# Performance work log

Hardware: AMD Instinct MI355X
Metric: run time of the kernel (lower is better)

The kernel has to match this reference:

```python
import jax, jax.numpy as jnp
import numpy as np

E = 768      # embed_dim (hidden_size)
H = 12       # num_attention_heads
DH = E // H  # head_dim = 64
B, S = 8, 1024


def setup_inputs() -> dict:
    key = jax.random.key(0)
    ks = jax.random.split(key, 10)
    sc = 1.0 / np.sqrt(E)
    inp = {
        "hidden_state": jax.random.normal(ks[0], (B, S, E), dtype=jnp.float32),
        # per-head Q/K/V projections, stacked over heads: [H, E, DH]
        "Wq": jax.random.normal(ks[1], (H, E, DH), dtype=jnp.float32) * sc,
        "bq": jax.random.normal(ks[2], (H, DH), dtype=jnp.float32) * 0.02,
        "Wk": jax.random.normal(ks[3], (H, E, DH), dtype=jnp.float32) * sc,
        "bk": jax.random.normal(ks[4], (H, DH), dtype=jnp.float32) * 0.02,
        "Wv": jax.random.normal(ks[5], (H, E, DH), dtype=jnp.float32) * sc,
        "bv": jax.random.normal(ks[6], (H, DH), dtype=jnp.float32) * 0.02,
        # output projection: [E, E]
        "Wo": jax.random.normal(ks[7], (E, E), dtype=jnp.float32) * sc,
        "bo": jax.random.normal(ks[8], (E,), dtype=jnp.float32) * 0.02,
    }
    return inp


def reference(hidden_state, Wq, bq, Wk, bk, Wv, bv, Wo, bo):
    # Q/K/V per head: [B,S,E] x [H,E,D] -> [B,H,S,D]
    q = jnp.einsum("bse,hed->bhsd", hidden_state, Wq) + bq[None, :, None, :]
    k = jnp.einsum("bse,hed->bhsd", hidden_state, Wk) + bk[None, :, None, :]
    v = jnp.einsum("bse,hed->bhsd", hidden_state, Wv) + bv[None, :, None, :]
    scale = 1.0 / jnp.sqrt(jnp.asarray(DH, dtype=q.dtype))
    scores = jnp.einsum("bhsd,bhtd->bhst", q, k) * scale   # [B,H,S,S]
    weights = jax.nn.softmax(scores, axis=-1)
    attn = jnp.einsum("bhst,bhtd->bhsd", weights, v)        # [B,H,S,D]
    # concat heads (head order matches ModuleList concat): [B,S,H*D]=[B,S,E]
    x = attn.transpose(0, 2, 1, 3).reshape(hidden_state.shape[0], hidden_state.shape[1], E)
    return x @ Wo + bo
```

## Files before the change

kernel.cpp:

```cpp
#include <hip/hip_runtime.h>

typedef unsigned short u16;
typedef __bf16 bf16;
typedef bf16 bf16x8 __attribute__((ext_vector_type(8)));
typedef float f32x4 __attribute__((ext_vector_type(4)));
typedef u16 u16x4 __attribute__((ext_vector_type(4)));
typedef u16 u16x8 __attribute__((ext_vector_type(8)));

#define MROWS 8192
#define EDIM 768
#define NQKV 2304
#define NHEAD 12
#define DH 64
#define SEQ 1024
#define BATCH 8
#define BH 96
#define BHSD (BH * SEQ * DH)
#define KIT64 (EDIM / 64)

#if __has_builtin(__builtin_amdgcn_exp2f)
#define EXP2(x) __builtin_amdgcn_exp2f(x)
#else
#define EXP2(x) exp2f(x)
#endif

__device__ __forceinline__ u16 f2bf(float f) {
  bf16 b = (bf16)f;
  return __builtin_bit_cast(u16, b);
}


__global__ void cvt_x(const float* __restrict__ x, u16* __restrict__ xb, int n) {
  int i = (blockIdx.x * blockDim.x + threadIdx.x) * 4;
  if (i >= n) return;
  float4 v = *(const float4*)(x + i);
  u16x4 o;
  o[0] = f2bf(v.x); o[1] = f2bf(v.y); o[2] = f2bf(v.z); o[3] = f2bf(v.w);
  *(u16x4*)(xb + i) = o;
}

__global__ __launch_bounds__(256) void pack_w(
    const float* __restrict__ Wq, const float* __restrict__ Wk,
    const float* __restrict__ Wv, const float* __restrict__ Wo,
    u16* __restrict__ Wt, u16* __restrict__ Wot) {
  __shared__ float T[64][65];
  int bid = blockIdx.x;
  int tid = threadIdx.x;
  int c = tid & 63, r4 = tid >> 6;
  if (bid < 432) {
    int region = bid / 144, rem = bid - region * 144;
    int h = rem / 12, e0 = (rem - h * 12) * 64;
    const float* W = region == 0 ? Wq : (region == 1 ? Wk : Wv);
    for (int p = 0; p < 16; p++) {
      int er = r4 + p * 4;
      T[er][c] = W[(size_t)(h * EDIM + e0 + er) * DH + c];
    }
    __syncthreads();
    int nbase = region * EDIM + h * 64;
    for (int p = 0; p < 16; p++) {
      int dr = r4 + p * 4;
      Wt[(size_t)(nbase + dr) * EDIM + e0 + c] = f2bf(T[c][dr]);
    }
  } else {
    bid -= 432;
    int n0 = (bid / 12) * 64, e0 = (bid - (bid / 12) * 12) * 64;
    for (int p = 0; p < 16; p++) {
      int er = r4 + p * 4;
      T[er][c] = Wo[(size_t)(e0 + er) * EDIM + n0 + c];
    }
    __syncthreads();
    for (int p = 0; p < 16; p++) {
      int dr = r4 + p * 4;
      Wot[(size_t)(n0 + dr) * EDIM + e0 + c] = f2bf(T[c][dr]);
    }
  }
}

__device__ __forceinline__ void gemm_core64(
    const u16* __restrict__ A, const u16* __restrict__ Bt,
    u16* As, u16* Bs,
    int m0, int n0, int tid, f32x4 acc[4][4]) {
  int wv = __builtin_amdgcn_readfirstlane(tid >> 6);
  int lane = tid & 63, quad = lane >> 4, l16 = lane & 15;
  int wm = (wv & 1) * 64, wn = (wv >> 1) * 64;
  int srow = tid >> 1;
  int cb = (tid & 1) * 4;
  const u16* Ag = A + (size_t)(m0 + srow) * EDIM + cb * 8;
  const u16* Bg = Bt + (size_t)(n0 + srow) * EDIM + cb * 8;
  int wbase = srow * 64;

  u16x8 ra[4], rb[4];
  for (int q = 0; q < 4; q++) {
    ra[q] = *(const u16x8*)(Ag + q * 8);
    rb[q] = *(const u16x8*)(Bg + q * 8);
  }
  for (int k = 0; k < KIT64; k++) {
    __syncthreads();
    for (int q = 0; q < 4; q++) {
      int sc = (((cb + q) ^ (srow & 7))) * 8;
      *(u16x8*)(As + wbase + sc) = ra[q];
      *(u16x8*)(Bs + wbase + sc) = rb[q];
    }
    __syncthreads();
    if (k + 1 < KIT64) {
      int ko = (k + 1) * 64;
      for (int q = 0; q < 4; q++) {
        ra[q] = *(const u16x8*)(Ag + ko + q * 8);
        rb[q] = *(const u16x8*)(Bg + ko + q * 8);
      }
    }
    for (int kh = 0; kh < 2; kh++) {
      bf16x8 af[4], bfr[4];
      for (int i = 0; i < 4; i++) {
        int row = wm + i * 16 + l16;
        af[i] = *(const bf16x8*)(As + row * 64 + (((kh * 4 + quad) ^ (row & 7))) * 8);
      }
      for (int j = 0; j < 4; j++) {
        int row = wn + j * 16 + l16;
        bfr[j] = *(const bf16x8*)(Bs + row * 64 + (((kh * 4 + quad) ^ (row & 7))) * 8);
      }
      for (int i = 0; i < 4; i++)
        for (int j = 0; j < 4; j++)
          acc[i][j] = __builtin_amdgcn_mfma_f32_16x16x32_bf16(af[i], bfr[j], acc[i][j], 0, 0, 0);
    }
  }
}

__global__ __launch_bounds__(256, 3) void gemm_qkv(
    const u16* __restrict__ A, const u16* __restrict__ Bt,
    const float* __restrict__ bq, const float* __restrict__ bk, const float* __restrict__ bv,
    u16* __restrict__ qkv) {
  __shared__ u16 As[128 * 64];
  __shared__ u16 Bs[128 * 64];
  int tid = threadIdx.x;
  int wv = tid >> 6, lane = tid & 63, quad = lane >> 4, l16 = lane & 15;
  int wm = (wv & 1) * 64, wn = (wv >> 1) * 64;
  int m0 = blockIdx.x * 128, n0 = blockIdx.y * 128;
  f32x4 acc[4][4] = {};
  gemm_core64(A, Bt, As, Bs, m0, n0, tid, acc);

  const float kQscale = 0.18033688011112042f;
  for (int i = 0; i < 4; i++) {
    int row0 = m0 + wm + i * 16 + quad * 4;
    for (int j = 0; j < 4; j++) {
      int n = n0 + wn + j * 16 + l16;
      int region = n / EDIM;
      int hd = n - region * EDIM;
      int h = hd >> 6, d = hd & 63;
      const float* bp = region == 0 ? bq : (region == 1 ? bk : bv);
      float bias = bp[hd];
      float scale = region == 0 ? kQscale : 1.0f;
      for (int r = 0; r < 4; r++) {
        int rr = row0 + r;
        int bb = rr >> 10, s = rr & 1023;
        float val = (acc[i][j][r] + bias) * scale;
        u16 bv16 = f2bf(val);
        int bhh = bb * NHEAD + h;
        if (region < 2) {
          qkv[(size_t)region * BHSD + ((size_t)bhh * SEQ + s) * DH + d] = bv16;
        } else {
          qkv[(size_t)2 * BHSD + ((size_t)bhh * DH + d) * SEQ + s] = bv16;
        }
      }
    }
  }
}

__global__ __launch_bounds__(256, 4) void attn_kernel(const u16* __restrict__ qkv, u16* __restrict__ attn) {
  int bh = blockIdx.x;
  int b = bh / NHEAD, h = bh - b * NHEAD;
  const u16* Q  = qkv + (size_t)bh * SEQ * DH;
  const u16* K  = qkv + (size_t)(BH + bh) * SEQ * DH;
  const u16* VT = qkv + (size_t)(2 * BH + bh) * SEQ * DH;
  int tid = threadIdx.x, wave = tid >> 6, lane = tid & 63, quad = lane >> 4, l16 = lane & 15;
  int q_base = blockIdx.y * 64 + wave * 16;

  __shared__ u16 Ks[64 * 72];
  __shared__ u16 Vts[80 * 72];
  __shared__ u16 Ps[4][16 * 72];

  for (int i = tid; i < 16 * 64; i += 256) {
    int rr = i >> 6, cc = i & 63;
    Vts[(64 + rr) * 72 + cc] = (rr == 0) ? (u16)0x3F80 : (u16)0;
  }

  bf16x8 qf[2];
  for (int c = 0; c < 2; c++)
    qf[c] = *(const bf16x8*)(Q + (size_t)(q_base + l16) * DH + c * 32 + quad * 8);

  f32x4 o[4] = {};
  f32x4 o5 = {};

  int tr = tid >> 3, tc8 = (tid & 7) * 8;

  u16x8 kv0 = *(const u16x8*)(K + (size_t)tr * DH + tc8);
  u16x8 kv1 = *(const u16x8*)(K + (size_t)(32 + tr) * DH + tc8);
  u16x8 vv0 = *(const u16x8*)(VT + (size_t)tr * SEQ + tc8);
  u16x8 vv1 = *(const u16x8*)(VT + (size_t)(32 + tr) * SEQ + tc8);

  for (int t0 = 0; t0 < SEQ; t0 += 64) {
    __syncthreads();
    *(u16x8*)(Ks + tr * 72 + tc8) = kv0;
    *(u16x8*)(Ks + (tr + 32) * 72 + tc8) = kv1;
    *(u16x8*)(Vts + tr * 72 + tc8) = vv0;
    *(u16x8*)(Vts + (tr + 32) * 72 + tc8) = vv1;
    __syncthreads();
    if (t0 + 64 < SEQ) {
      kv0 = *(const u16x8*)(K + (size_t)(t0 + 64 + tr) * DH + tc8);
      kv1 = *(const u16x8*)(K + (size_t)(t0 + 96 + tr) * DH + tc8);
      vv0 = *(const u16x8*)(VT + (size_t)tr * SEQ + t0 + 64 + tc8);
      vv1 = *(const u16x8*)(VT + (size_t)(32 + tr) * SEQ + t0 + 64 + tc8);
    }

    float p[4][4];
    for (int tc = 0; tc < 4; tc++) {
      bf16x8 kf0 = *(const bf16x8*)(Ks + (tc * 16 + l16) * 72 + quad * 8);
      bf16x8 kf1 = *(const bf16x8*)(Ks + (tc * 16 + l16) * 72 + 32 + quad * 8);
      f32x4 z = {};
      z = __builtin_amdgcn_mfma_f32_16x16x32_bf16(qf[0], kf0, z, 0, 0, 0);
      z = __builtin_amdgcn_mfma_f32_16x16x32_bf16(qf[1], kf1, z, 0, 0, 0);
      for (int r = 0; r < 4; r++)
        p[tc][r] = EXP2(z[r]);
    }

    u16* P = Ps[wave];
    for (int tc = 0; tc < 4; tc++)
      for (int r = 0; r < 4; r++)
        P[(quad * 4 + r) * 72 + tc * 16 + l16] = f2bf(p[tc][r]);
    bf16x8 pf[2];
    for (int kc = 0; kc < 2; kc++)
      pf[kc] = *(const bf16x8*)(P + l16 * 72 + kc * 32 + quad * 8);

    for (int n = 0; n < 4; n++) {
      bf16x8 vf0 = *(const bf16x8*)(Vts + (n * 16 + l16) * 72 + quad * 8);
      bf16x8 vf1 = *(const bf16x8*)(Vts + (n * 16 + l16) * 72 + 32 + quad * 8);
      o[n] = __builtin_amdgcn_mfma_f32_16x16x32_bf16(pf[0], vf0, o[n], 0, 0, 0);
      o[n] = __builtin_amdgcn_mfma_f32_16x16x32_bf16(pf[1], vf1, o[n], 0, 0, 0);
    }
    bf16x8 v50 = *(const bf16x8*)(Vts + (64 + l16) * 72 + quad * 8);
    bf16x8 v51 = *(const bf16x8*)(Vts + (64 + l16) * 72 + 32 + quad * 8);
    o5 = __builtin_amdgcn_mfma_f32_16x16x32_bf16(pf[0], v50, o5, 0, 0, 0);
    o5 = __builtin_amdgcn_mfma_f32_16x16x32_bf16(pf[1], v51, o5, 0, 0, 0);
  }

  for (int r = 0; r < 4; r++) {
    float s = __shfl(o5[r], quad << 4);
    float inv = 1.0f / s;
    int qrow = q_base + quad * 4 + r;
    size_t rowoff = (size_t)(b * SEQ + qrow) * EDIM + h * DH;
    for (int n = 0; n < 4; n++)
      attn[rowoff + n * 16 + l16] = f2bf(o[n][r] * inv);
  }
}

__global__ __launch_bounds__(256, 3) void gemm_out(
    const u16* __restrict__ A, const u16* __restrict__ Bt,
    const float* __restrict__ bo, float* __restrict__ out) {
  __shared__ u16 As[128 * 64];
  __shared__ u16 Bs[128 * 64];
  int tid = threadIdx.x;
  int wv = tid >> 6, lane = tid & 63, quad = lane >> 4, l16 = lane & 15;
  int wm = (wv & 1) * 64, wn = (wv >> 1) * 64;
  int m0 = blockIdx.x * 128, n0 = blockIdx.y * 128;
  f32x4 acc[4][4] = {};
  gemm_core64(A, Bt, As, Bs, m0, n0, tid, acc);

  for (int i = 0; i < 4; i++) {
    int row0 = m0 + wm + i * 16 + quad * 4;
    for (int j = 0; j < 4; j++) {
      int n = n0 + wn + j * 16 + l16;
      float bias = bo[n];
      for (int r = 0; r < 4; r++)
        out[(size_t)(row0 + r) * EDIM + n] = acc[i][j][r] + bias;
    }
  }
}

extern "C" void kernel_launch(void* const* d_in, const int* in_sizes, int n_in,
                              void* d_out, int out_size, void* d_ws, size_t ws_size,
                              hipStream_t stream) {
  const float* x  = (const float*)d_in[0];
  const float* Wq = (const float*)d_in[1];
  const float* bq = (const float*)d_in[2];
  const float* Wk = (const float*)d_in[3];
  const float* bk = (const float*)d_in[4];
  const float* Wv = (const float*)d_in[5];
  const float* bv = (const float*)d_in[6];
  const float* Wo = (const float*)d_in[7];
  const float* bo = (const float*)d_in[8];
  float* out = (float*)d_out;
  char* ws = (char*)d_ws;

  u16* Xb   = (u16*)(ws);
  u16* Wt   = (u16*)(ws + 12582912);
  u16* Wot  = (u16*)(ws + 16121856);
  u16* qkv  = (u16*)(ws + 17301504);
  u16* attn = (u16*)(ws + 55050240);

  cvt_x<<<6144, 256, 0, stream>>>(x, Xb, MROWS * EDIM);
  pack_w<<<576, 256, 0, stream>>>(Wq, Wk, Wv, Wo, Wt, Wot);
  gemm_qkv<<<dim3(64, 18), 256, 0, stream>>>(Xb, Wt, bq, bk, bv, qkv);
  attn_kernel<<<dim3(96, 16), 256, 0, stream>>>(qkv, attn);
  gemm_out<<<dim3(64, 6), 256, 0, stream>>>(attn, Wot, bo, out);
}
```

Measured before the change: 217.4 us.

## Use direct global-to-LDS loads in GEMM core and raise occupancy bound

Replaces the register-staged global loads and explicit LDS stores in the shared GEMM core with global_load_lds instructions that write 16-byte chunks straight into swizzled LDS. The source column is swizzled instead of the destination so the existing XOR-swizzled fragment reads stay valid. This frees staging registers, which pairs with raising the launch bounds from 3 to 4 blocks per CU. The price is losing the overlap of next-tile prefetch with MFMA work, since loads are now issued and waited on within the same iteration between barriers.

After: 218.1 us. Within noise of the previous version (+0.3%).

```diff
diff --git a/kernel.cpp b/kernel.cpp
--- a/kernel.cpp
+++ b/kernel.cpp
@@ -27,6 +27,12 @@
 __device__ __forceinline__ u16 f2bf(float f) {
   bf16 b = (bf16)f;
   return __builtin_bit_cast(u16, b);
+}
+
+__device__ __forceinline__ void gload_lds16(const u16* g, u16* l) {
+  __builtin_amdgcn_global_load_lds(
+      (const __attribute__((address_space(1))) void*)g,
+      (__attribute__((address_space(3))) void*)l, 16, 0, 0);
 }
 
 
@@ -83,32 +89,24 @@
   int wv = __builtin_amdgcn_readfirstlane(tid >> 6);
   int lane = tid & 63, quad = lane >> 4, l16 = lane & 15;
   int wm = (wv & 1) * 64, wn = (wv >> 1) * 64;
-  int srow = tid >> 1;
-  int cb = (tid & 1) * 4;
-  const u16* Ag = A + (size_t)(m0 + srow) * EDIM + cb * 8;
-  const u16* Bg = Bt + (size_t)(n0 + srow) * EDIM + cb * 8;
-  int wbase = srow * 64;
-
-  u16x8 ra[4], rb[4];
-  for (int q = 0; q < 4; q++) {
-    ra[q] = *(const u16x8*)(Ag + q * 8);
-    rb[q] = *(const u16x8*)(Bg + q * 8);
-  }
+  int lr = lane >> 3, cpos = lane & 7;
+  int swcol = (cpos ^ lr) * 8;
+  const u16* Ag = A + (size_t)(m0 + wv * 32 + lr) * EDIM + swcol;
+  const u16* Bg = Bt + (size_t)(n0 + wv * 32 + lr) * EDIM + swcol;
+  u16* Asl = As + (wv * 32 + lr) * 64 + cpos * 8;
+  u16* Bsl = Bs + (wv * 32 + lr) * 64 + cpos * 8;
+
   for (int k = 0; k < KIT64; k++) {
     __syncthreads();
+    const u16* ak = Ag + k * 64;
+    const u16* bk = Bg + k * 64;
+#pragma unroll
     for (int q = 0; q < 4; q++) {
-      int sc = (((cb + q) ^ (srow & 7))) * 8;
-      *(u16x8*)(As + wbase + sc) = ra[q];
-      *(u16x8*)(Bs + wbase + sc) = rb[q];
-    }
-    __syncthreads();
-    if (k + 1 < KIT64) {
-      int ko = (k + 1) * 64;
-      for (int q = 0; q < 4; q++) {
-        ra[q] = *(const u16x8*)(Ag + ko + q * 8);
-        rb[q] = *(const u16x8*)(Bg + ko + q * 8);
-      }
-    }
+      gload_lds16(ak + q * 8 * EDIM, Asl + q * 512);
+      gload_lds16(bk + q * 8 * EDIM, Bsl + q * 512);
+    }
+    __syncthreads();
+#pragma unroll
     for (int kh = 0; kh < 2; kh++) {
       bf16x8 af[4], bfr[4];
       for (int i = 0; i < 4; i++) {
@@ -126,12 +124,12 @@
   }
 }
 
-__global__ __launch_bounds__(256, 3) void gemm_qkv(
+__global__ __launch_bounds__(256, 4) void gemm_qkv(
     const u16* __restrict__ A, const u16* __restrict__ Bt,
     const float* __restrict__ bq, const float* __restrict__ bk, const float* __restrict__ bv,
     u16* __restrict__ qkv) {
-  __shared__ u16 As[128 * 64];
-  __shared__ u16 Bs[128 * 64];
+  __shared__ __align__(16) u16 As[128 * 64];
+  __shared__ __align__(16) u16 Bs[128 * 64];
   int tid = threadIdx.x;
   int wv = tid >> 6, lane = tid & 63, quad = lane >> 4, l16 = lane & 15;
   int wm = (wv & 1) * 64, wn = (wv >> 1) * 64;
@@ -253,11 +251,11 @@
   }
 }
 
-__global__ __launch_bounds__(256, 3) void gemm_out(
+__global__ __launch_bounds__(256, 4) void gemm_out(
     const u16* __restrict__ A, const u16* __restrict__ Bt,
     const float* __restrict__ bo, float* __restrict__ out) {
-  __shared__ u16 As[128 * 64];
-  __shared__ u16 Bs[128 * 64];
+  __shared__ __align__(16) u16 As[128 * 64];
+  __shared__ __align__(16) u16 Bs[128 * 64];
   int tid = threadIdx.x;
   int wv = tid >> 6, lane = tid & 63, quad = lane >> 4, l16 = lane & 15;
   int wm = (wv & 1) * 64, wn = (wv >> 1) * 64;
```
